# Performance work log

Hardware: AMD Instinct MI355X
Metric: run time of the kernel (lower is better)

## Reference

```python
import jax, jax.numpy as jnp
import numpy as np

N_NODES = 50000
N_RELS = 20          # raw relations; enriched total = 2*N_RELS + 1
N_EDGES = 500000
EMB = 16
N_CLASSES = 16
N_BASES = 40


def setup_inputs() -> dict:
    key = jax.random.key(0)
    ks = jax.random.split(key, 8)
    R_tot = 2 * N_RELS + 1
    src = jax.random.randint(ks[0], (N_EDGES,), 0, N_NODES)
    dst = jax.random.randint(ks[1], (N_EDGES,), 0, N_NODES)
    rel = jax.random.randint(ks[2], (N_EDGES,), 0, N_RELS)
    scale = 0.05
    comps1 = jax.random.normal(ks[3], (R_tot, N_BASES), jnp.float32) * scale
    bases1 = jax.random.normal(ks[4], (N_BASES, N_NODES, EMB), jnp.float32) * scale
    comps2 = jax.random.normal(ks[5], (R_tot, N_BASES), jnp.float32) * scale
    bases2 = jax.random.normal(ks[6], (N_BASES, EMB, N_CLASSES), jnp.float32) * scale
    bias1 = jnp.zeros((EMB,), jnp.float32)
    bias2 = jnp.zeros((N_CLASSES,), jnp.float32)
    return {"src": src, "dst": dst, "rel": rel,
            "comps1": comps1, "bases1": bases1,
            "comps2": comps2, "bases2": bases2,
            "bias1": bias1, "bias2": bias2}


def reference(src, dst, rel, comps1, bases1, comps2, bases2, bias1, bias2):
    N = bases1.shape[1]
    emb = bases1.shape[2]
    R_tot = comps1.shape[0]
    R = (R_tot - 1) // 2

    # enrich: originals + inverses + self-loops (relation 2R)
    loop = jnp.arange(N)
    s = jnp.concatenate([src, dst, loop])           # [E_tot]
    o = jnp.concatenate([dst, src, loop])
    r = jnp.concatenate([rel, rel + R, jnp.full((N,), 2 * R, rel.dtype)])

    # row-normalization of the vertical graph: value = 1 / count(row = r*N + s)
    seg = r * N + s
    cnt = jax.ops.segment_sum(jnp.ones_like(s, jnp.float32), seg,
                              num_segments=R_tot * N)
    v = 1.0 / cnt[seg]                               # [E_tot]

    # layer 1: basis-decomposed weights [R_tot, N, emb]
    w1 = jnp.einsum('rb,bne->rne', comps1, bases1)
    # hor_graph @ w1.view(R*N, emb): h[s] += v * w1[r, o]
    h = jnp.zeros((N, emb), w1.dtype).at[s].add(v[:, None] * w1[r, o])
    h = jax.nn.relu(h + bias1)

    # ver_graph @ h: hv[r, s] += v * h[o]  -> [R_tot, N, emb]
    hv = jnp.zeros((R_tot, N, emb), h.dtype).at[r, s].add(v[:, None] * h[o])

    # layer 2: basis-decomposed weights [R_tot, emb, C]; bmm + sum over relations
    w2 = jnp.einsum('rb,bec->rec', comps2, bases2)
    out = jnp.einsum('rne,rec->nc', hv, w2) + bias2  # [N, C]
    return out
```

## Files before the change

### kernel.cpp

```cpp
#include <hip/hip_runtime.h>

#define N_NODES 50000
#define N_RELSR 20
#define R_TOT   41
#define N_EDGES 500000
#define EMB     16
#define NCLS    16
#define NB      40
#define E_TOT   (2 * N_EDGES + N_NODES)
#define NE_COL  (N_NODES * EMB)
#define NBLK_N  ((N_NODES + 255) / 256)

__device__ __forceinline__ unsigned short f2bf(float f) {
    unsigned u = __float_as_uint(f);
    u += 0x7FFFu + ((u >> 16) & 1u);
    return (unsigned short)(u >> 16);
}

__device__ __forceinline__ void edge_decode(int i, const int* __restrict__ src,
                                            const int* __restrict__ dst,
                                            const int* __restrict__ rel,
                                            int& s, int& o, int& r) {
    if (i < N_EDGES) {
        s = src[i]; o = dst[i]; r = rel[i];
    } else if (i < 2 * N_EDGES) {
        int j = i - N_EDGES;
        s = dst[j]; o = src[j]; r = rel[j] + N_RELSR;
    } else {
        int n = i - 2 * N_EDGES;
        s = n; o = n; r = 2 * N_RELSR;
    }
}


__global__ void k_count(const int* __restrict__ src, const int* __restrict__ dst,
                        const int* __restrict__ rel, int2* __restrict__ cnt2,
                        int* __restrict__ rank) {
    int i = blockIdx.x * blockDim.x + threadIdx.x;
    if (i >= E_TOT) return;
    int s, o, r;
    edge_decode(i, src, dst, rel, s, o, r);
    rank[i] = atomicAdd(&cnt2[r * N_NODES + s].x, 1);
}

__global__ void k_degA(int2* __restrict__ cnt2, int* __restrict__ deg,
                       int* __restrict__ bsum) {
    __shared__ int red[256];
    int t = threadIdx.x;
    int s = blockIdx.x * 256 + t;
    int run = 0;
    if (s < N_NODES) {
        for (int r = 0; r < R_TOT; r++) {
            int idx = r * N_NODES + s;
            int2 val = cnt2[idx];
            val.y = run;
            cnt2[idx] = val;
            run += val.x;
        }
        deg[s] = run;
    }
    red[t] = run;
    __syncthreads();
    for (int st = 128; st > 0; st >>= 1) {
        if (t < st) red[t] += red[t + st];
        __syncthreads();
    }
    if (t == 0) bsum[blockIdx.x] = red[0];
}

__global__ void k_degB(int* __restrict__ bsum) {
    __shared__ int sh[256];
    int t = threadIdx.x;
    int v = (t < NBLK_N) ? bsum[t] : 0;
    sh[t] = v;
    __syncthreads();
    for (int d = 1; d < 256; d <<= 1) {
        int x = (t >= d) ? sh[t - d] : 0;
        __syncthreads();
        sh[t] += x;
        __syncthreads();
    }
    if (t < NBLK_N) bsum[t] = sh[t] - v;
}

__global__ void k_degC(const int* __restrict__ deg, const int* __restrict__ bsum,
                       int* __restrict__ off) {
    __shared__ int sh[256];
    int t = threadIdx.x;
    int s = blockIdx.x * 256 + t;
    int d = (s < N_NODES) ? deg[s] : 0;
    sh[t] = d;
    __syncthreads();
    for (int dd = 1; dd < 256; dd <<= 1) {
        int x = (t >= dd) ? sh[t - dd] : 0;
        __syncthreads();
        sh[t] += x;
        __syncthreads();
    }
    int excl = sh[t] - d + bsum[blockIdx.x];
    if (s < N_NODES) off[s] = excl;
    if (s == 0) off[N_NODES] = E_TOT;
}

__global__ void k_fill(const int* __restrict__ src, const int* __restrict__ dst,
                       const int* __restrict__ rel, const int2* __restrict__ cnt2,
                       const int* __restrict__ rank, const int* __restrict__ off,
                       int2* __restrict__ recs) {
    int i = blockIdx.x * blockDim.x + threadIdx.x;
    if (i >= E_TOT) return;
    int s, o, r;
    edge_decode(i, src, dst, rel, s, o, r);
    int2 cr = cnt2[r * N_NODES + s];
    float v = 1.0f / (float)cr.x;
    recs[off[s] + cr.y + rank[i]] = make_int2((r << 16) | o, __float_as_int(v));
}

template<int RT>
__device__ __forceinline__ void w1_pass(const float* __restrict__ comps1,
                                        const float4* __restrict__ b4,
                                        uint2* __restrict__ w1p2, int j4, int r0) {
    float4 acc[RT];
#pragma unroll
    for (int r = 0; r < RT; r++) { acc[r].x = 0.f; acc[r].y = 0.f; acc[r].z = 0.f; acc[r].w = 0.f; }
    for (int b = 0; b < NB; b++) {
        float4 bb = b4[(size_t)b * (NE_COL / 4) + j4];
#pragma unroll
        for (int r = 0; r < RT; r++) {
            float cc = comps1[(r0 + r) * NB + b];
            acc[r].x = fmaf(cc, bb.x, acc[r].x);
            acc[r].y = fmaf(cc, bb.y, acc[r].y);
            acc[r].z = fmaf(cc, bb.z, acc[r].z);
            acc[r].w = fmaf(cc, bb.w, acc[r].w);
        }
    }
#pragma unroll
    for (int r = 0; r < RT; r++) {
        uint2 pk;
        pk.x = ((unsigned)f2bf(acc[r].y) << 16) | (unsigned)f2bf(acc[r].x);
        pk.y = ((unsigned)f2bf(acc[r].w) << 16) | (unsigned)f2bf(acc[r].z);
        w1p2[(size_t)(r0 + r) * (NE_COL / 4) + j4] = pk;
    }
}

__global__ void __launch_bounds__(256, 2)
k_w1(const float* __restrict__ comps1, const float* __restrict__ bases1,
     uint2* __restrict__ w1p2) {
    int j4 = blockIdx.x * blockDim.x + threadIdx.x;
    if (j4 >= NE_COL / 4) return;
    const float4* b4 = (const float4*)bases1;
    w1_pass<14>(comps1, b4, w1p2, j4, 0);
    w1_pass<14>(comps1, b4, w1p2, j4, 14);
    w1_pass<13>(comps1, b4, w1p2, j4, 28);
}

__global__ void k_w2(const float* __restrict__ comps2, const float* __restrict__ bases2,
                     float* __restrict__ w2t) {
    int r = blockIdx.x;
    int t = threadIdx.x;
    int c = t >> 4, e = t & 15;
    float acc = 0.f;
#pragma unroll 8
    for (int b = 0; b < NB; b++) acc += comps2[r * NB + b] * bases2[b * (EMB * NCLS) + e * NCLS + c];
    w2t[r * (EMB * NCLS) + t] = acc;
}

__global__ void k_l1_gather(const int* __restrict__ off, const int2* __restrict__ recs,
                            const unsigned* __restrict__ w1p,
                            const float* __restrict__ bias1, float* __restrict__ h) {
    int t = blockIdx.x * blockDim.x + threadIdx.x;
    if (t >= N_NODES * 8) return;
    int s = t >> 3, e2 = t & 7;
    int beg = off[s], end = off[s + 1];
    float ax = 0.f, ay = 0.f;
    int j = beg;
    for (; j + 3 < end; j += 4) {
        int2 r0 = recs[j], r1 = recs[j + 1], r2 = recs[j + 2], r3 = recs[j + 3];
        unsigned p0 = w1p[(size_t)(r0.x >> 16) * (NE_COL / 2) + (r0.x & 0xFFFF) * 8 + e2];
        unsigned p1 = w1p[(size_t)(r1.x >> 16) * (NE_COL / 2) + (r1.x & 0xFFFF) * 8 + e2];
        unsigned p2 = w1p[(size_t)(r2.x >> 16) * (NE_COL / 2) + (r2.x & 0xFFFF) * 8 + e2];
        unsigned p3 = w1p[(size_t)(r3.x >> 16) * (NE_COL / 2) + (r3.x & 0xFFFF) * 8 + e2];
        float v0 = __int_as_float(r0.y), v1 = __int_as_float(r1.y);
        float v2 = __int_as_float(r2.y), v3 = __int_as_float(r3.y);
        ax = fmaf(v0, __uint_as_float(p0 << 16), ax);
        ay = fmaf(v0, __uint_as_float(p0 & 0xFFFF0000u), ay);
        ax = fmaf(v1, __uint_as_float(p1 << 16), ax);
        ay = fmaf(v1, __uint_as_float(p1 & 0xFFFF0000u), ay);
        ax = fmaf(v2, __uint_as_float(p2 << 16), ax);
        ay = fmaf(v2, __uint_as_float(p2 & 0xFFFF0000u), ay);
        ax = fmaf(v3, __uint_as_float(p3 << 16), ax);
        ay = fmaf(v3, __uint_as_float(p3 & 0xFFFF0000u), ay);
    }
    for (; j < end; j++) {
        int2 rc = recs[j];
        unsigned p = w1p[(size_t)(rc.x >> 16) * (NE_COL / 2) + (rc.x & 0xFFFF) * 8 + e2];
        float v = __int_as_float(rc.y);
        ax = fmaf(v, __uint_as_float(p << 16), ax);
        ay = fmaf(v, __uint_as_float(p & 0xFFFF0000u), ay);
    }
    float2 res;
    res.x = fmaxf(ax + bias1[2 * e2], 0.f);
    res.y = fmaxf(ay + bias1[2 * e2 + 1], 0.f);
    ((float2*)h)[t] = res;
}

__global__ void k_l1_gather_fly(const int* __restrict__ off, const int2* __restrict__ recs,
                                const float* __restrict__ comps1,
                                const float* __restrict__ bases1,
                                const float* __restrict__ bias1, float* __restrict__ h) {
    __shared__ float c1[R_TOT * NB];
    for (int q = threadIdx.x; q < R_TOT * NB; q += blockDim.x) c1[q] = comps1[q];
    __syncthreads();
    int t = blockIdx.x * blockDim.x + threadIdx.x;
    int s = t >> 4, e = t & 15;
    int beg = off[s], end = off[s + 1];
    float acc = 0.f;
    for (int j = beg; j < end; j++) {
        int2 rec = recs[j];
        int o = rec.x & 0xFFFF, r = rec.x >> 16;
        float v = __int_as_float(rec.y);
        const float* cr = &c1[r * NB];
        float w = 0.f;
#pragma unroll 8
        for (int b = 0; b < NB; b++) w += cr[b] * bases1[(size_t)b * NE_COL + o * EMB + e];
        acc += v * w;
    }
    h[t] = fmaxf(acc + bias1[e], 0.f);
}

#define W2C 20
#define W2R (16 * W2C + 4)
__global__ void k_l2_gather(const int* __restrict__ off, const int2* __restrict__ recs,
                            const float* __restrict__ h, const float* __restrict__ w2t,
                            const float* __restrict__ bias2, float* __restrict__ out) {
    __shared__ __align__(16) float w2s[R_TOT * W2R];
    for (int q = threadIdx.x; q < R_TOT * (EMB * NCLS); q += blockDim.x) {
        int r = q >> 8;
        int x = q & 255;
        int c = x >> 4, e = x & 15;
        w2s[r * W2R + c * W2C + e] = w2t[q];
    }
    __syncthreads();
    int t = blockIdx.x * blockDim.x + threadIdx.x;
    if (t >= NE_COL) return;
    int s = t >> 4, c = t & 15;
    int beg = off[s], end = off[s + 1];
    int cbase = c * W2C;
    float acc = 0.f;
    int j = beg;
    for (; j + 1 < end; j += 2) {
        int2 ra = recs[j], rb = recs[j + 1];
        const float4* ha = (const float4*)(h + (size_t)(ra.x & 0xFFFF) * EMB);
        const float4* hb = (const float4*)(h + (size_t)(rb.x & 0xFFFF) * EMB);
        float4 h0 = ha[0], h1 = ha[1], h2 = ha[2], h3 = ha[3];
        float4 g0 = hb[0], g1 = hb[1], g2 = hb[2], g3 = hb[3];
        const float4* wa = (const float4*)&w2s[(ra.x >> 16) * W2R + cbase];
        const float4* wb = (const float4*)&w2s[(rb.x >> 16) * W2R + cbase];
        float4 a0 = wa[0], a1 = wa[1], a2 = wa[2], a3 = wa[3];
        float4 b0 = wb[0], b1 = wb[1], b2 = wb[2], b3 = wb[3];
        float da, db;
        da  = h0.x * a0.x; da = fmaf(h0.y, a0.y, da); da = fmaf(h0.z, a0.z, da); da = fmaf(h0.w, a0.w, da);
        da = fmaf(h1.x, a1.x, da); da = fmaf(h1.y, a1.y, da); da = fmaf(h1.z, a1.z, da); da = fmaf(h1.w, a1.w, da);
        da = fmaf(h2.x, a2.x, da); da = fmaf(h2.y, a2.y, da); da = fmaf(h2.z, a2.z, da); da = fmaf(h2.w, a2.w, da);
        da = fmaf(h3.x, a3.x, da); da = fmaf(h3.y, a3.y, da); da = fmaf(h3.z, a3.z, da); da = fmaf(h3.w, a3.w, da);
        db  = g0.x * b0.x; db = fmaf(g0.y, b0.y, db); db = fmaf(g0.z, b0.z, db); db = fmaf(g0.w, b0.w, db);
        db = fmaf(g1.x, b1.x, db); db = fmaf(g1.y, b1.y, db); db = fmaf(g1.z, b1.z, db); db = fmaf(g1.w, b1.w, db);
        db = fmaf(g2.x, b2.x, db); db = fmaf(g2.y, b2.y, db); db = fmaf(g2.z, b2.z, db); db = fmaf(g2.w, b2.w, db);
        db = fmaf(g3.x, b3.x, db); db = fmaf(g3.y, b3.y, db); db = fmaf(g3.z, b3.z, db); db = fmaf(g3.w, b3.w, db);
        acc = fmaf(__int_as_float(ra.y), da, acc);
        acc = fmaf(__int_as_float(rb.y), db, acc);
    }
    for (; j < end; j++) {
        int2 ra = recs[j];
        const float4* ha = (const float4*)(h + (size_t)(ra.x & 0xFFFF) * EMB);
        float4 h0 = ha[0], h1 = ha[1], h2 = ha[2], h3 = ha[3];
        const float4* wa = (const float4*)&w2s[(ra.x >> 16) * W2R + cbase];
        float4 a0 = wa[0], a1 = wa[1], a2 = wa[2], a3 = wa[3];
        float da;
        da  = h0.x * a0.x; da = fmaf(h0.y, a0.y, da); da = fmaf(h0.z, a0.z, da); da = fmaf(h0.w, a0.w, da);
        da = fmaf(h1.x, a1.x, da); da = fmaf(h1.y, a1.y, da); da = fmaf(h1.z, a1.z, da); da = fmaf(h1.w, a1.w, da);
        da = fmaf(h2.x, a2.x, da); da = fmaf(h2.y, a2.y, da); da = fmaf(h2.z, a2.z, da); da = fmaf(h2.w, a2.w, da);
        da = fmaf(h3.x, a3.x, da); da = fmaf(h3.y, a3.y, da); da = fmaf(h3.z, a3.z, da); da = fmaf(h3.w, a3.w, da);
        acc = fmaf(__int_as_float(ra.y), da, acc);
    }
    out[s * NCLS + c] = acc + bias2[c];
}

static inline size_t align64(size_t x) { return (x + 63) & ~(size_t)63; }

extern "C" void kernel_launch(void* const* d_in, const int* in_sizes, int n_in,
                              void* d_out, int out_size, void* d_ws, size_t ws_size,
                              hipStream_t stream) {
    const int*   src    = (const int*)d_in[0];
    const int*   dst    = (const int*)d_in[1];
    const int*   rel    = (const int*)d_in[2];
    const float* comps1 = (const float*)d_in[3];
    const float* bases1 = (const float*)d_in[4];
    const float* comps2 = (const float*)d_in[5];
    const float* bases2 = (const float*)d_in[6];
    const float* bias1  = (const float*)d_in[7];
    const float* bias2  = (const float*)d_in[8];
    float* out = (float*)d_out;
    (void)in_sizes; (void)n_in; (void)out_size;

    char* ws = (char*)d_ws;
    size_t off_b = 0;
    unsigned short* w1 = (unsigned short*)ws;
    int2*  cnt2 = (int2*)ws;
    int*   rank = (int*)(ws + align64((size_t)R_TOT * N_NODES * 8));
    off_b = align64((size_t)R_TOT * NE_COL * 2);
    int*   deg  = (int*)(ws + off_b);  off_b = align64(off_b + (size_t)N_NODES * 4);
    int*   off  = (int*)(ws + off_b);  off_b = align64(off_b + (size_t)(N_NODES + 1) * 4);
    int*   bsum = (int*)(ws + off_b);  off_b = align64(off_b + (size_t)256 * 4);
    int2*  recs = (int2*)(ws + off_b); off_b = align64(off_b + (size_t)E_TOT * 8);
    float* h    = (float*)(ws + off_b); off_b = align64(off_b + (size_t)NE_COL * 4);
    float* w2t  = (float*)(ws + off_b); off_b = align64(off_b + (size_t)R_TOT * EMB * NCLS * 4);
    const bool materialize_w1 = (ws_size >= off_b);
    if (!materialize_w1) {
        off_b = 0;
        cnt2 = (int2*)(ws + off_b);  off_b = align64(off_b + (size_t)R_TOT * N_NODES * 8);
        rank = (int*)(ws + off_b);   off_b = align64(off_b + (size_t)E_TOT * 4);
        deg  = (int*)(ws + off_b);   off_b = align64(off_b + (size_t)N_NODES * 4);
        off  = (int*)(ws + off_b);   off_b = align64(off_b + (size_t)(N_NODES + 1) * 4);
        bsum = (int*)(ws + off_b);   off_b = align64(off_b + (size_t)256 * 4);
        recs = (int2*)(ws + off_b);  off_b = align64(off_b + (size_t)E_TOT * 8);
        h    = (float*)(ws + off_b); off_b = align64(off_b + (size_t)NE_COL * 4);
        w2t  = (float*)(ws + off_b); off_b = align64(off_b + (size_t)R_TOT * EMB * NCLS * 4);
    }

    hipMemsetAsync(cnt2, 0, (size_t)R_TOT * N_NODES * 8, stream);

    const int BLK = 256;
    const int g_edge = (E_TOT + BLK - 1) / BLK;
    const int g_w1   = (NE_COL / 4 + BLK - 1) / BLK;
    const int g_l1   = (N_NODES * 8 + BLK - 1) / BLK;
    const int g_l1f  = (N_NODES * 16) / BLK;
    const int g_l2   = (NE_COL + 511) / 512;

    k_count<<<g_edge, BLK, 0, stream>>>(src, dst, rel, cnt2, rank);
    k_degA<<<NBLK_N, 256, 0, stream>>>(cnt2, deg, bsum);
    k_degB<<<1, 256, 0, stream>>>(bsum);
    k_degC<<<NBLK_N, 256, 0, stream>>>(deg, bsum, off);
    k_fill<<<g_edge, BLK, 0, stream>>>(src, dst, rel, cnt2, rank, off, recs);
    k_w2<<<R_TOT, EMB * NCLS, 0, stream>>>(comps2, bases2, w2t);

    if (materialize_w1) {
        k_w1<<<g_w1, BLK, 0, stream>>>(comps1, bases1, (uint2*)w1);
        k_l1_gather<<<g_l1, BLK, 0, stream>>>(off, recs, (const unsigned*)w1, bias1, h);
    } else {
        k_l1_gather_fly<<<g_l1f, BLK, 0, stream>>>(off, recs, comps1, bases1, bias1, h);
    }

    k_l2_gather<<<g_l2, 512, 0, stream>>>(off, recs, h, w2t, bias2, out);
}
```

Measured before the change: 427.3 us.

## Stage bases1 tile in LDS so k_w1 reads each basis value once

The w1 materialization kernel now loads a 40x64 float4 tile of bases1 and all of comps1 into shared memory. Eight waves then split the 41 relations between them, each computing 5 or 6 relations from the shared tile. Previously each thread made three passes over all 40 bases, reading bases1 from global memory three times. The new version reads bases1 once, at the cost of about 46KB of LDS per 512-thread block and lower occupancy.

After: 444.0 us. +3.9%, slower.

```diff
diff --git a/kernel.cpp b/kernel.cpp
--- a/kernel.cpp
+++ b/kernel.cpp
@@ -115,42 +115,47 @@
     recs[off[s] + cr.y + rank[i]] = make_int2((r << 16) | o, __float_as_int(v));
 }
 
-template<int RT>
-__device__ __forceinline__ void w1_pass(const float* __restrict__ comps1,
-                                        const float4* __restrict__ b4,
-                                        uint2* __restrict__ w1p2, int j4, int r0) {
-    float4 acc[RT];
-#pragma unroll
-    for (int r = 0; r < RT; r++) { acc[r].x = 0.f; acc[r].y = 0.f; acc[r].z = 0.f; acc[r].w = 0.f; }
-    for (int b = 0; b < NB; b++) {
-        float4 bb = b4[(size_t)b * (NE_COL / 4) + j4];
-#pragma unroll
-        for (int r = 0; r < RT; r++) {
-            float cc = comps1[(r0 + r) * NB + b];
-            acc[r].x = fmaf(cc, bb.x, acc[r].x);
-            acc[r].y = fmaf(cc, bb.y, acc[r].y);
-            acc[r].z = fmaf(cc, bb.z, acc[r].z);
-            acc[r].w = fmaf(cc, bb.w, acc[r].w);
-        }
-    }
-#pragma unroll
-    for (int r = 0; r < RT; r++) {
-        uint2 pk;
-        pk.x = ((unsigned)f2bf(acc[r].y) << 16) | (unsigned)f2bf(acc[r].x);
-        pk.y = ((unsigned)f2bf(acc[r].w) << 16) | (unsigned)f2bf(acc[r].z);
-        w1p2[(size_t)(r0 + r) * (NE_COL / 4) + j4] = pk;
-    }
-}
-
-__global__ void __launch_bounds__(256, 2)
+#define W1_COLS 64
+__global__ void __launch_bounds__(512, 1)
 k_w1(const float* __restrict__ comps1, const float* __restrict__ bases1,
      uint2* __restrict__ w1p2) {
-    int j4 = blockIdx.x * blockDim.x + threadIdx.x;
-    if (j4 >= NE_COL / 4) return;
+    __shared__ float4 tile[NB][W1_COLS];
+    __shared__ float  c1s[R_TOT * NB];
+    int tid = threadIdx.x;
+    for (int q = tid; q < R_TOT * NB; q += 512) c1s[q] = comps1[q];
+    int j4base = blockIdx.x * W1_COLS;
     const float4* b4 = (const float4*)bases1;
-    w1_pass<14>(comps1, b4, w1p2, j4, 0);
-    w1_pass<14>(comps1, b4, w1p2, j4, 14);
-    w1_pass<13>(comps1, b4, w1p2, j4, 28);
+    for (int q = tid; q < NB * W1_COLS; q += 512) {
+        int b = q >> 6, jc = q & 63;
+        tile[b][jc] = b4[(size_t)b * (NE_COL / 4) + j4base + jc];
+    }
+    __syncthreads();
+    int wave = tid >> 6, lane = tid & 63;
+    int r0 = wave * 5;
+    int nr = (wave == 7) ? 6 : 5;
+    float4 acc[6];
+#pragma unroll
+    for (int k = 0; k < 6; k++) { acc[k].x = 0.f; acc[k].y = 0.f; acc[k].z = 0.f; acc[k].w = 0.f; }
+    for (int b = 0; b < NB; b++) {
+        float4 bb = tile[b][lane];
+#pragma unroll
+        for (int k = 0; k < 6; k++) {
+            float cc = c1s[(r0 + k) * NB + b];
+            acc[k].x = fmaf(cc, bb.x, acc[k].x);
+            acc[k].y = fmaf(cc, bb.y, acc[k].y);
+            acc[k].z = fmaf(cc, bb.z, acc[k].z);
+            acc[k].w = fmaf(cc, bb.w, acc[k].w);
+        }
+    }
+#pragma unroll
+    for (int k = 0; k < 6; k++) {
+        if (k < nr) {
+            uint2 pk;
+            pk.x = ((unsigned)f2bf(acc[k].y) << 16) | (unsigned)f2bf(acc[k].x);
+            pk.y = ((unsigned)f2bf(acc[k].w) << 16) | (unsigned)f2bf(acc[k].z);
+            w1p2[(size_t)(r0 + k) * (NE_COL / 4) + j4base + lane] = pk;
+        }
+    }
 }
 
 __global__ void k_w2(const float* __restrict__ comps2, const float* __restrict__ bases2,
@@ -331,7 +336,7 @@
 
     const int BLK = 256;
     const int g_edge = (E_TOT + BLK - 1) / BLK;
-    const int g_w1   = (NE_COL / 4 + BLK - 1) / BLK;
+    const int g_w1   = (NE_COL / 4) / W1_COLS;
     const int g_l1   = (N_NODES * 8 + BLK - 1) / BLK;
     const int g_l1f  = (N_NODES * 16) / BLK;
     const int g_l2   = (NE_COL + 511) / 512;
@@ -344,7 +349,7 @@
     k_w2<<<R_TOT, EMB * NCLS, 0, stream>>>(comps2, bases2, w2t);
 
     if (materialize_w1) {
-        k_w1<<<g_w1, BLK, 0, stream>>>(comps1, bases1, (uint2*)w1);
+        k_w1<<<g_w1, 512, 0, stream>>>(comps1, bases1, (uint2*)w1);
         k_l1_gather<<<g_l1, BLK, 0, stream>>>(off, recs, (const unsigned*)w1, bias1, h);
     } else {
         k_l1_gather_fly<<<g_l1f, BLK, 0, stream>>>(off, recs, comps1, bases1, bias1, h);
```
